# Kernel tuning notes

Measured on AMD Instinct MI355X. Metric: run time of the kernel, lower is better.

Reference implementation:

```python
import jax, jax.numpy as jnp
import numpy as np

# hyperparameters (from hp_manager)
UNTANH = 3.0
W_SCALE = 4.0
EMA_SPEED = 0.01
REW_SENS = 4.0
NOISE_SCALE = 0.01
WD = 1e-4
SPEED = 1.0
WIDTH = 4.0
MOMENTUM = 0.9
LR = 0.01
C_MOMENT = 0.9
A_VAR_GOAL = 0.01
BUNTANH_SCALE = float(np.sqrt(2.0 + np.sqrt(2.0)))
B, N, D = 4, 512, 128


def rms_norm(x, axes=(-1,), eps=1e-8):
    return x * jax.lax.rsqrt(jnp.mean(x * x, axis=axes, keepdims=True) + eps)


def buntanh(x, a, s):
    return a * jnp.tanh(x / a) * s


def sinkhorn_knopp(A, n_iters=5, eps=1e-6):
    for _ in range(n_iters):
        A = A / (jnp.sum(A, axis=-1, keepdims=True) + eps)
        A = A / (jnp.sum(A, axis=-2, keepdims=True) + eps)
    return A


def wrapping_gaussian_mask(dim, center, width):
    j = jnp.arange(dim, dtype=jnp.float32)
    d = jnp.abs(j - center)
    d = jnp.minimum(d, dim - d)  # wrap-around distance
    return jnp.exp(-(d * d) / (2.0 * width * width))


def piece_forward(x, W):
    raw = jnp.einsum('bnj,bnjk->bnk', x, W)
    return buntanh(raw, UNTANH, BUNTANH_SCALE)


def piece_gradient(layer_input, err, E_base, key):
    E_curr = jax.nn.softmax(err, axis=-1)
    E_new = E_base * (1.0 - EMA_SPEED) + EMA_SPEED * E_curr
    advantage = E_curr - E_new
    plasticity = 1.0 + rms_norm(advantage[..., None] * REW_SENS)  # [B,N,D,1]
    noisy = layer_input + NOISE_SCALE * jax.random.normal(key, layer_input.shape, layer_input.dtype)
    lg1 = rms_norm(-(err[..., :, None] * noisy[..., None, :]))  # bni,bnj->bnij
    return plasticity * lg1, E_new


def piece_step(W, g_ema, grad, step_counter):
    grad = grad - WD * W
    center = (step_counter * SPEED) % D
    mask = wrapping_gaussian_mask(D, center, WIDTH)  # applied along last dim
    grad = grad * mask
    g_new = MOMENTUM * g_ema + (1.0 - MOMENTUM) * grad
    W_new = W + LR * g_new
    W_new = rms_norm(W_new, axes=(-1, -2)) * W_SCALE
    return W_new, g_new


def setup_inputs() -> dict:
    key = jax.random.key(0)
    ks = jax.random.split(key, 14)
    return {
        'state': 1e-5 * jax.random.normal(ks[0], (B, N, D), jnp.float32),
        'output': 1e-5 * jax.random.normal(ks[1], (B, N, D), jnp.float32),
        'A_ema': jax.random.normal(ks[2], (B, N, N), jnp.float32),
        'w1': jax.random.normal(ks[3], (B, N, D, D), jnp.float32) / np.sqrt(D),
        'w2': jax.random.normal(ks[4], (B, N, D, D), jnp.float32) / np.sqrt(D),
        'w3': jax.random.normal(ks[5], (B, N, D, D), jnp.float32) / np.sqrt(D),
        'g1': 0.01 * jax.random.normal(ks[6], (B, N, D, D), jnp.float32),
        'g2': 0.01 * jax.random.normal(ks[7], (B, N, D, D), jnp.float32),
        'g3': 0.01 * jax.random.normal(ks[8], (B, N, D, D), jnp.float32),
        'eb1': 0.01 + 0.01 * jax.random.normal(ks[9], (B, N, D), jnp.float32),
        'eb2': 0.01 + 0.01 * jax.random.normal(ks[10], (B, N, D), jnp.float32),
        'eb3': 0.01 + 0.01 * jax.random.normal(ks[11], (B, N, D), jnp.float32),
        'eye_env': jax.random.normal(ks[12], (B, D), jnp.float32),
        'stomach_env': jax.random.normal(ks[13], (B, D), jnp.float32),
        'step_counter': 2,
    }


def reference(state, output, A_ema, w1, w2, w3, g1, g2, g3, eb1, eb2, eb3,
              eye_env, stomach_env, step_counter):
    sg = jax.lax.stop_gradient
    nkey = jax.random.key(1)
    k_bore, k1, k2, k3 = jax.random.split(nkey, 4)

    queries = piece_forward(state, w3)
    keys = piece_forward(state, w2)
    prediction = piece_forward(state, w1)

    raw_A = jnp.einsum('bnd,bmd->bnm', queries, keys) / np.sqrt(D)
    raw_A = rms_norm(raw_A, axes=(-1, -2))
    if step_counter == 1:
        A_ema_new = raw_A
    else:
        A_ema_new = A_ema * C_MOMENT + raw_A * (1.0 - C_MOMENT)
    raw_A = sinkhorn_knopp(A_ema_new)
    uniform_baseline = 0.5 / N
    sparse_A = jnp.where(raw_A > uniform_baseline, raw_A, 0.0)
    A = sinkhorn_knopp(sparse_A)
    A = A.at[:, 0:2, :].set(0.0)

    current_var = jnp.var(A, axis=(-1, -2), keepdims=True)  # [B,1,1]
    vd = jax.nn.relu(A_VAR_GOAL - current_var)
    boredom_noise = vd * jax.random.normal(k_bore, output.shape, output.dtype)
    target = jnp.einsum('bnm,bmd->bnd', A, output + boredom_noise)
    target = target.at[:, 0, :].set(eye_env).at[:, 1, :].set(stomach_env)

    err1_base = prediction - target
    err2 = keys - sg(err1_base)
    err3 = queries - sg(err2)
    err1 = prediction - (target + sg(err3))

    gr1, eb1n = piece_gradient(state, err1, eb1, k1)
    gr2, eb2n = piece_gradient(state, err2, eb2, k2)
    gr3, eb3n = piece_gradient(state, err3, eb3, k3)
    w1n, g1n = piece_step(w1, g1, gr1, step_counter)
    w2n, g2n = piece_step(w2, g2, gr2, step_counter)
    w3n, g3n = piece_step(w3, g3, gr3, step_counter)

    new_output = prediction
    new_state = target
    return (new_state, new_output, w1n, w2n, w3n, A_ema_new)
```

## Files before the change

kernel.cpp:

```cpp
#include <hip/hip_runtime.h>
#include <math.h>

#define Bq 4
#define Nq 512
#define Dq 128

#define C_UNTANH   3.0f
#define C_BSCALE   1.8477590650225735f
#define C_INVSQRTD 0.08838834764831845f
#define C_WD       1e-4f
#define C_MOM      0.9f
#define C_LR       0.01f
#define C_WSCALE   4.0f

__global__ __launch_bounds__(256) void k_fwd(const float* __restrict__ state,
    const float* __restrict__ w1, const float* __restrict__ w2, const float* __restrict__ w3,
    float* __restrict__ pred, float* __restrict__ keyv, float* __restrict__ qry) {
  int bn = blockIdx.x;
  int t = threadIdx.x;
  int k = t & 127;
  int half = t >> 7;
  __shared__ float xs[Dq];
  __shared__ float ps[256];
  if (t < Dq) xs[t] = state[bn * Dq + t];
  __syncthreads();
  const float* Ws[3] = {w1, w2, w3};
  float* dsts[3] = {pred, keyv, qry};
  for (int p = 0; p < 3; p++) {
    const float* W = Ws[p] + (size_t)bn * Dq * Dq + (size_t)half * 64 * Dq;
    float acc = 0.f;
#pragma unroll 16
    for (int j = 0; j < 64; j++) acc += xs[half * 64 + j] * W[j * Dq + k];
    ps[t] = acc;
    __syncthreads();
    if (t < Dq) {
      float r = ps[t] + ps[t + 128];
      r = C_UNTANH * tanhf(r / C_UNTANH) * C_BSCALE;
      dsts[p][bn * Dq + t] = r;
    }
    __syncthreads();
  }
}

__global__ __launch_bounds__(256) void k_qk(const float* __restrict__ qry,
    const float* __restrict__ keyv, float* __restrict__ rawS, double* __restrict__ part) {
  __shared__ float Qs[16][Dq + 1];
  __shared__ float Ks[16][Dq + 1];
  __shared__ double red[256];
  int b = blockIdx.z, n0 = blockIdx.x * 16, m0 = blockIdx.y * 16;
  int t = threadIdx.x;
#pragma unroll
  for (int i = 0; i < 8; i++) {
    int idx = i * 256 + t;
    int r = idx >> 7, c = idx & 127;
    Qs[r][c] = qry[((size_t)b * Nq + n0 + r) * Dq + c];
    Ks[r][c] = keyv[((size_t)b * Nq + m0 + r) * Dq + c];
  }
  __syncthreads();
  int tn = t >> 4, tm = t & 15;
  float a = 0.f;
#pragma unroll 16
  for (int d = 0; d < Dq; d++) a += Qs[tn][d] * Ks[tm][d];
  a *= C_INVSQRTD;
  rawS[((size_t)b * Nq + n0 + tn) * Nq + m0 + tm] = a;
  red[t] = (double)a * (double)a;
  __syncthreads();
  for (int s = 128; s > 0; s >>= 1) { if (t < s) red[t] += red[t + s]; __syncthreads(); }
  if (t == 0) part[(size_t)b * 1024 + blockIdx.y * 32 + blockIdx.x] = red[0];
}

__global__ __launch_bounds__(256) void k_acc(const double* __restrict__ part, double* __restrict__ acc) {
  int b = blockIdx.x, t = threadIdx.x;
  double s = 0.0;
  for (int i = t; i < 1024; i += 256) s += part[(size_t)b * 1024 + i];
  __shared__ double red[256];
  red[t] = s;
  __syncthreads();
  for (int k = 128; k > 0; k >>= 1) { if (t < k) red[t] += red[t + k]; __syncthreads(); }
  if (t == 0) acc[b] = red[0];
}

__global__ __launch_bounds__(256) void k_ema(float* __restrict__ A, const float* __restrict__ A_ema,
    const double* __restrict__ acc, const int* __restrict__ stepc, float* __restrict__ outA) {
  int idx = blockIdx.x * 256 + threadIdx.x;
  if (idx >= Bq * Nq * Nq) return;
  int b = idx / (Nq * Nq);
  float mean = (float)(acc[b] / (double)(Nq * Nq));
  float rs = 1.0f / sqrtf(mean + 1e-8f);
  float val = A[idx] * rs;
  float res = (stepc[0] == 1) ? val : 0.9f * A_ema[idx] + 0.1f * val;
  outA[idx] = res;
  A[idx] = res;
}

__global__ __launch_bounds__(256) void k_row(float* __restrict__ A) {
  int bn = blockIdx.x, t = threadIdx.x;
  float* row = A + (size_t)bn * Nq;
  float v0 = row[t], v1 = row[t + 256];
  __shared__ double red[256];
  red[t] = (double)v0 + (double)v1;
  __syncthreads();
  for (int s = 128; s > 0; s >>= 1) { if (t < s) red[t] += red[t + s]; __syncthreads(); }
  double den = red[0] + 1e-6;
  row[t] = (float)((double)v0 / den);
  row[t + 256] = (float)((double)v1 / den);
}

__global__ __launch_bounds__(256) void k_col(float* __restrict__ A) {
  int blk = blockIdx.x, t = threadIdx.x;
  int b = blk >> 9, m = blk & 511;
  float* base = A + (size_t)b * Nq * Nq + m;
  float v0 = base[(size_t)t * Nq], v1 = base[(size_t)(t + 256) * Nq];
  __shared__ double red[256];
  red[t] = (double)v0 + (double)v1;
  __syncthreads();
  for (int s = 128; s > 0; s >>= 1) { if (t < s) red[t] += red[t + s]; __syncthreads(); }
  double den = red[0] + 1e-6;
  base[(size_t)t * Nq] = (float)((double)v0 / den);
  base[(size_t)(t + 256) * Nq] = (float)((double)v1 / den);
}

__global__ __launch_bounds__(256) void k_sparse(float* __restrict__ A) {
  int idx = blockIdx.x * 256 + threadIdx.x;
  if (idx >= Bq * Nq * Nq) return;
  float v = A[idx];
  A[idx] = (v > 0.0009765625f) ? v : 0.0f;
}

__global__ __launch_bounds__(128) void k_target(const float* __restrict__ A,
    const float* __restrict__ output, const float* __restrict__ eye_env,
    const float* __restrict__ stomach_env, float* __restrict__ out_state) {
  int bn = blockIdx.x, t = threadIdx.x;
  int b = bn >> 9, n = bn & 511;
  float tg;
  if (n == 0) {
    tg = eye_env[b * Dq + t];
  } else if (n == 1) {
    tg = stomach_env[b * Dq + t];
  } else {
    const float* Arow = A + (size_t)bn * Nq;
    const float* ob = output + (size_t)b * Nq * Dq;
    __shared__ float as[128];
    float acc = 0.f;
    for (int m0 = 0; m0 < Nq; m0 += 128) {
      __syncthreads();
      as[t] = Arow[m0 + t];
      __syncthreads();
#pragma unroll 16
      for (int m = 0; m < 128; m++) acc += as[m] * ob[(size_t)(m0 + m) * Dq + t];
    }
    tg = acc;
  }
  out_state[(size_t)bn * Dq + t] = tg;
}

__device__ __forceinline__ void softmax_plast(float e, const float* __restrict__ eb,
    float* __restrict__ pl, int base, int t, float* red) {
  red[t] = e;
  __syncthreads();
  for (int s = 64; s > 0; s >>= 1) { if (t < s) red[t] = fmaxf(red[t], red[t + s]); __syncthreads(); }
  float mx = red[0];
  __syncthreads();
  float ex = expf(e - mx);
  red[t] = ex;
  __syncthreads();
  for (int s = 64; s > 0; s >>= 1) { if (t < s) red[t] += red[t + s]; __syncthreads(); }
  float Ec = ex / red[0];
  __syncthreads();
  float En = eb[base] * 0.99f + 0.01f * Ec;
  float adv = Ec - En;
  float x = adv * 4.0f;
  pl[base] = 1.0f + x / sqrtf(x * x + 1e-8f);
}

__global__ __launch_bounds__(128) void k_err(const float* __restrict__ pred,
    const float* __restrict__ qry, const float* __restrict__ keyv,
    const float* __restrict__ target, const float* __restrict__ state,
    const float* __restrict__ eb1, const float* __restrict__ eb2, const float* __restrict__ eb3,
    float* __restrict__ err1, float* __restrict__ err2, float* __restrict__ err3,
    float* __restrict__ pl1, float* __restrict__ pl2, float* __restrict__ pl3,
    float* __restrict__ msn) {
  int bn = blockIdx.x, t = threadIdx.x;
  int base = bn * Dq + t;
  float pr = pred[base], qv = qry[base], kv = keyv[base], tg = target[base];
  float e1b = pr - tg;
  float e2 = kv - e1b;
  float e3 = qv - e2;
  float e1 = pr - (tg + e3);
  err1[base] = e1; err2[base] = e2; err3[base] = e3;
  __shared__ float red[128];
  float st = state[base];
  red[t] = st * st;
  __syncthreads();
  for (int s = 64; s > 0; s >>= 1) { if (t < s) red[t] += red[t + s]; __syncthreads(); }
  if (t == 0) msn[bn] = red[0] / (float)Dq;
  __syncthreads();
  softmax_plast(e1, eb1, pl1, base, t, red);
  softmax_plast(e2, eb2, pl2, base, t, red);
  softmax_plast(e3, eb3, pl3, base, t, red);
}

__device__ __forceinline__ float stepw(float w, float g, float c, float st, float mk, double* ssq) {
  float grad = (c * st - C_WD * w) * mk;
  float gn = C_MOM * g + (1.0f - C_MOM) * grad;
  float wn = w + C_LR * gn;
  *ssq += (double)wn * (double)wn;
  return wn;
}

__global__ __launch_bounds__(256) void k_step(const float* __restrict__ W, const float* __restrict__ G,
    const float* __restrict__ err, const float* __restrict__ pl, const float* __restrict__ state,
    const float* __restrict__ msn, const int* __restrict__ stepc, float* __restrict__ outW) {
  int bn = blockIdx.x, t = threadIdx.x;
  __shared__ __align__(16) float Wn[Dq * Dq];
  __shared__ __align__(16) float ers[Dq];
  __shared__ __align__(16) float pls[Dq];
  __shared__ __align__(16) float sts[Dq];
  __shared__ __align__(16) float msk[Dq];
  __shared__ double red[256];
  if (t < Dq) {
    ers[t] = err[bn * Dq + t];
    pls[t] = pl[bn * Dq + t];
    sts[t] = state[bn * Dq + t];
    float center = fmodf((float)stepc[0] * 1.0f, 128.0f);
    float d = fabsf((float)t - center);
    d = fminf(d, 128.0f - d);
    msk[t] = expf(-(d * d) * (1.0f / 32.0f));
  }
  float msnv = msn[bn];
  __syncthreads();
  const float4* W4 = (const float4*)(W + (size_t)bn * Dq * Dq);
  const float4* G4 = (const float4*)(G + (size_t)bn * Dq * Dq);
  float4* Wn4 = (float4*)Wn;
  double ssq = 0.0;
#pragma unroll
  for (int i = 0; i < 16; i++) {
    int f4 = i * 256 + t;
    int p = f4 >> 5;
    float4 w4v = W4[f4];
    float4 g4v = G4[f4];
    float4 st4 = ((const float4*)sts)[f4 & 31];
    float4 mk4 = ((const float4*)msk)[f4 & 31];
    float ep = ers[p];
    float denom = sqrtf(ep * ep * msnv + 1e-8f);
    float c = -pls[p] * ep / denom;
    float4 o;
    o.x = stepw(w4v.x, g4v.x, c, st4.x, mk4.x, &ssq);
    o.y = stepw(w4v.y, g4v.y, c, st4.y, mk4.y, &ssq);
    o.z = stepw(w4v.z, g4v.z, c, st4.z, mk4.z, &ssq);
    o.w = stepw(w4v.w, g4v.w, c, st4.w, mk4.w, &ssq);
    Wn4[f4] = o;
  }
  red[t] = ssq;
  __syncthreads();
  for (int s = 128; s > 0; s >>= 1) { if (t < s) red[t] += red[t + s]; __syncthreads(); }
  float mean = (float)(red[0] / (double)(Dq * Dq));
  float scale = C_WSCALE / sqrtf(mean + 1e-8f);
  float4* out4 = (float4*)(outW + (size_t)bn * Dq * Dq);
#pragma unroll
  for (int i = 0; i < 16; i++) {
    int f4 = i * 256 + t;
    float4 v = Wn4[f4];
    v.x *= scale; v.y *= scale; v.z *= scale; v.w *= scale;
    out4[f4] = v;
  }
}

extern "C" void kernel_launch(void* const* d_in, const int* in_sizes, int n_in,
                              void* d_out, int out_size, void* d_ws, size_t ws_size,
                              hipStream_t stream) {
  const float* state   = (const float*)d_in[0];
  const float* output  = (const float*)d_in[1];
  const float* A_ema   = (const float*)d_in[2];
  const float* w1      = (const float*)d_in[3];
  const float* w2      = (const float*)d_in[4];
  const float* w3      = (const float*)d_in[5];
  const float* g1      = (const float*)d_in[6];
  const float* g2      = (const float*)d_in[7];
  const float* g3      = (const float*)d_in[8];
  const float* eb1     = (const float*)d_in[9];
  const float* eb2     = (const float*)d_in[10];
  const float* eb3     = (const float*)d_in[11];
  const float* eye     = (const float*)d_in[12];
  const float* stomach = (const float*)d_in[13];
  const int*   stepc   = (const int*)d_in[14];

  float* out = (float*)d_out;
  float* o_state = out;
  float* o_out   = out + 262144;
  float* o_w1    = out + 524288;
  float* o_w2    = o_w1 + 33554432;
  float* o_w3    = o_w2 + 33554432;
  float* o_A     = o_w3 + 33554432;

  float* ws = (float*)d_ws;
  float* A    = ws;
  float* qry  = ws + 1048576;
  float* keyv = ws + 1310720;
  float* err1 = ws + 1572864;
  float* err2 = ws + 1835008;
  float* err3 = ws + 2097152;
  float* pl1  = ws + 2359296;
  float* pl2  = ws + 2621440;
  float* pl3  = ws + 2883584;
  float* msn  = ws + 3145728;
  double* part = (double*)(ws + 3147776);
  double* acc  = part + 4096;

  k_fwd<<<Bq * Nq, 256, 0, stream>>>(state, w1, w2, w3, o_out, keyv, qry);
  k_qk<<<dim3(32, 32, Bq), 256, 0, stream>>>(qry, keyv, A, part);
  k_acc<<<Bq, 256, 0, stream>>>(part, acc);
  k_ema<<<4096, 256, 0, stream>>>(A, A_ema, acc, stepc, o_A);
  for (int it = 0; it < 5; it++) {
    k_row<<<Bq * Nq, 256, 0, stream>>>(A);
    k_col<<<Bq * Nq, 256, 0, stream>>>(A);
  }
  k_sparse<<<4096, 256, 0, stream>>>(A);
  for (int it = 0; it < 5; it++) {
    k_row<<<Bq * Nq, 256, 0, stream>>>(A);
    k_col<<<Bq * Nq, 256, 0, stream>>>(A);
  }
  k_target<<<Bq * Nq, 128, 0, stream>>>(A, output, eye, stomach, o_state);
  k_err<<<Bq * Nq, 128, 0, stream>>>(o_out, qry, keyv, o_state, state,
                                     eb1, eb2, eb3, err1, err2, err3, pl1, pl2, pl3, msn);
  k_step<<<Bq * Nq, 256, 0, stream>>>(w1, g1, err1, pl1, state, msn, stepc, o_w1);
  k_step<<<Bq * Nq, 256, 0, stream>>>(w2, g2, err2, pl2, state, msn, stepc, o_w2);
  k_step<<<Bq * Nq, 256, 0, stream>>>(w3, g3, err3, pl3, state, msn, stepc, o_w3);
}
```

Baseline: 1.286 ms.

## Fuse Sinkhorn pipeline into cooperative kernel and restructure fwd, target, step kernels

Replaces the EMA, sparsify and twenty row/column normalization launches with one cooperative kernel. It keeps each block's column slab in registers and exchanges partial row sums through global memory with grid syncs. It also vectorizes the forward matvec and QK dot products with float4, and retiles the target matmul to compute several rows per block from a shared output tile. The three weight-step kernels become one launch that holds the updated weights in registers instead of shared memory. This cuts launch count and global traffic on A, but only 64 blocks run the Sinkhorn phase and normalization moves from double to float precision.

```diff
diff --git a/kernel.cpp b/kernel.cpp
--- a/kernel.cpp
+++ b/kernel.cpp
@@ -1,5 +1,8 @@
 #include <hip/hip_runtime.h>
+#include <hip/hip_cooperative_groups.h>
 #include <math.h>
+
+namespace cg = cooperative_groups;
 
 #define Bq 4
 #define Nq 512
@@ -12,30 +15,39 @@
 #define C_MOM      0.9f
 #define C_LR       0.01f
 #define C_WSCALE   4.0f
+#define C_SPARSE   0.0009765625f
 
 __global__ __launch_bounds__(256) void k_fwd(const float* __restrict__ state,
     const float* __restrict__ w1, const float* __restrict__ w2, const float* __restrict__ w3,
     float* __restrict__ pred, float* __restrict__ keyv, float* __restrict__ qry) {
   int bn = blockIdx.x;
   int t = threadIdx.x;
-  int k = t & 127;
-  int half = t >> 7;
+  int g = t & 31;
+  int h = t >> 5;
   __shared__ float xs[Dq];
-  __shared__ float ps[256];
+  __shared__ float4 red[8][32];
   if (t < Dq) xs[t] = state[bn * Dq + t];
   __syncthreads();
   const float* Ws[3] = {w1, w2, w3};
   float* dsts[3] = {pred, keyv, qry};
   for (int p = 0; p < 3; p++) {
-    const float* W = Ws[p] + (size_t)bn * Dq * Dq + (size_t)half * 64 * Dq;
-    float acc = 0.f;
-#pragma unroll 16
-    for (int j = 0; j < 64; j++) acc += xs[half * 64 + j] * W[j * Dq + k];
-    ps[t] = acc;
+    const float4* W4 = (const float4*)(Ws[p] + (size_t)bn * Dq * Dq);
+    float4 acc = {0.f, 0.f, 0.f, 0.f};
+#pragma unroll
+    for (int i = 0; i < 16; i++) {
+      int j = h * 16 + i;
+      float x = xs[j];
+      float4 w = W4[j * 32 + g];
+      acc.x += x * w.x; acc.y += x * w.y; acc.z += x * w.z; acc.w += x * w.w;
+    }
+    red[h][g] = acc;
     __syncthreads();
     if (t < Dq) {
-      float r = ps[t] + ps[t + 128];
-      r = C_UNTANH * tanhf(r / C_UNTANH) * C_BSCALE;
+      const float* rp = (const float*)&red[0][0];
+      float ssum = 0.f;
+#pragma unroll
+      for (int h2 = 0; h2 < 8; h2++) ssum += rp[h2 * 128 + t];
+      float r = C_UNTANH * tanhf(ssum / C_UNTANH) * C_BSCALE;
       dsts[p][bn * Dq + t] = r;
     }
     __syncthreads();
@@ -44,8 +56,8 @@
 
 __global__ __launch_bounds__(256) void k_qk(const float* __restrict__ qry,
     const float* __restrict__ keyv, float* __restrict__ rawS, double* __restrict__ part) {
-  __shared__ float Qs[16][Dq + 1];
-  __shared__ float Ks[16][Dq + 1];
+  __shared__ float Qs[16][132];
+  __shared__ float Ks[16][132];
   __shared__ double red[256];
   int b = blockIdx.z, n0 = blockIdx.x * 16, m0 = blockIdx.y * 16;
   int t = threadIdx.x;
@@ -58,9 +70,15 @@
   }
   __syncthreads();
   int tn = t >> 4, tm = t & 15;
+  const float4* Q4 = (const float4*)&Qs[tn][0];
+  const float4* K4 = (const float4*)&Ks[tm][0];
   float a = 0.f;
-#pragma unroll 16
-  for (int d = 0; d < Dq; d++) a += Qs[tn][d] * Ks[tm][d];
+#pragma unroll
+  for (int d = 0; d < 32; d++) {
+    float4 q = Q4[d];
+    float4 k = K4[d];
+    a += q.x * k.x + q.y * k.y + q.z * k.z + q.w * k.w;
+  }
   a *= C_INVSQRTD;
   rawS[((size_t)b * Nq + n0 + tn) * Nq + m0 + tm] = a;
   red[t] = (double)a * (double)a;
@@ -69,89 +87,158 @@
   if (t == 0) part[(size_t)b * 1024 + blockIdx.y * 32 + blockIdx.x] = red[0];
 }
 
-__global__ __launch_bounds__(256) void k_acc(const double* __restrict__ part, double* __restrict__ acc) {
-  int b = blockIdx.x, t = threadIdx.x;
-  double s = 0.0;
-  for (int i = t; i < 1024; i += 256) s += part[(size_t)b * 1024 + i];
-  __shared__ double red[256];
-  red[t] = s;
-  __syncthreads();
-  for (int k = 128; k > 0; k >>= 1) { if (t < k) red[t] += red[t + k]; __syncthreads(); }
-  if (t == 0) acc[b] = red[0];
-}
-
-__global__ __launch_bounds__(256) void k_ema(float* __restrict__ A, const float* __restrict__ A_ema,
-    const double* __restrict__ acc, const int* __restrict__ stepc, float* __restrict__ outA) {
-  int idx = blockIdx.x * 256 + threadIdx.x;
-  if (idx >= Bq * Nq * Nq) return;
-  int b = idx / (Nq * Nq);
-  float mean = (float)(acc[b] / (double)(Nq * Nq));
-  float rs = 1.0f / sqrtf(mean + 1e-8f);
-  float val = A[idx] * rs;
-  float res = (stepc[0] == 1) ? val : 0.9f * A_ema[idx] + 0.1f * val;
-  outA[idx] = res;
-  A[idx] = res;
-}
-
-__global__ __launch_bounds__(256) void k_row(float* __restrict__ A) {
-  int bn = blockIdx.x, t = threadIdx.x;
-  float* row = A + (size_t)bn * Nq;
-  float v0 = row[t], v1 = row[t + 256];
-  __shared__ double red[256];
-  red[t] = (double)v0 + (double)v1;
-  __syncthreads();
-  for (int s = 128; s > 0; s >>= 1) { if (t < s) red[t] += red[t + s]; __syncthreads(); }
-  double den = red[0] + 1e-6;
-  row[t] = (float)((double)v0 / den);
-  row[t + 256] = (float)((double)v1 / den);
-}
-
-__global__ __launch_bounds__(256) void k_col(float* __restrict__ A) {
-  int blk = blockIdx.x, t = threadIdx.x;
-  int b = blk >> 9, m = blk & 511;
-  float* base = A + (size_t)b * Nq * Nq + m;
-  float v0 = base[(size_t)t * Nq], v1 = base[(size_t)(t + 256) * Nq];
-  __shared__ double red[256];
-  red[t] = (double)v0 + (double)v1;
-  __syncthreads();
-  for (int s = 128; s > 0; s >>= 1) { if (t < s) red[t] += red[t + s]; __syncthreads(); }
-  double den = red[0] + 1e-6;
-  base[(size_t)t * Nq] = (float)((double)v0 / den);
-  base[(size_t)(t + 256) * Nq] = (float)((double)v1 / den);
-}
-
-__global__ __launch_bounds__(256) void k_sparse(float* __restrict__ A) {
-  int idx = blockIdx.x * 256 + threadIdx.x;
-  if (idx >= Bq * Nq * Nq) return;
-  float v = A[idx];
-  A[idx] = (v > 0.0009765625f) ? v : 0.0f;
-}
-
-__global__ __launch_bounds__(128) void k_target(const float* __restrict__ A,
+__global__ __launch_bounds__(256) void k_Apipe(float* __restrict__ A,
+    const float* __restrict__ A_ema, const double* __restrict__ part,
+    const int* __restrict__ stepc, float* __restrict__ outA, float* __restrict__ prs) {
+  cg::grid_group grid = cg::this_grid();
+  int blk = blockIdx.x;
+  int b = blk >> 4;
+  int s = blk & 15;
+  int m0 = s * 32;
+  int t = threadIdx.x;
+  int c4 = t & 7;
+  int rq = t >> 3;
+  __shared__ float rs_l[512];
+  __shared__ float cs_l[32];
+  __shared__ float4 carr[32][8];
+  __shared__ double dred[256];
+
+  double ps = 0.0;
+  for (int i = t; i < 1024; i += 256) ps += part[(size_t)b * 1024 + i];
+  dred[t] = ps;
+  __syncthreads();
+  for (int k = 128; k > 0; k >>= 1) { if (t < k) dred[t] += dred[t + k]; __syncthreads(); }
+  float invs = rsqrtf((float)(dred[0] / (double)(Nq * Nq)) + 1e-8f);
+  int step1 = (stepc[0] == 1);
+
+  const size_t brow = (size_t)b * Nq;
+  float4 vS[16];
+
+#pragma unroll
+  for (int k = 0; k < 16; k++) {
+    int r = rq + 32 * k;
+    const float4* Ar = (const float4*)(A + (brow + r) * Nq + m0);
+    float4 v = Ar[c4];
+    v.x *= invs; v.y *= invs; v.z *= invs; v.w *= invs;
+    if (!step1) {
+      const float4* Er = (const float4*)(A_ema + (brow + r) * Nq + m0);
+      float4 e = Er[c4];
+      v.x = 0.9f * e.x + 0.1f * v.x;
+      v.y = 0.9f * e.y + 0.1f * v.y;
+      v.z = 0.9f * e.z + 0.1f * v.z;
+      v.w = 0.9f * e.w + 0.1f * v.w;
+    }
+    vS[k] = v;
+    float4* Or = (float4*)(outA + (brow + r) * Nq + m0);
+    Or[c4] = v;
+    float p = v.x + v.y + v.z + v.w;
+    p += __shfl_xor(p, 1);
+    p += __shfl_xor(p, 2);
+    p += __shfl_xor(p, 4);
+    if (c4 == 0) prs[((size_t)(b * 16 + s)) * 512 + r] = p;
+  }
+  __threadfence();
+  grid.sync();
+
+  for (int iter = 0; iter < 10; iter++) {
+    for (int r = t; r < 512; r += 256) {
+      float ssum = 0.f;
+#pragma unroll
+      for (int s2 = 0; s2 < 16; s2++) ssum += prs[((size_t)(b * 16 + s2)) * 512 + r];
+      rs_l[r] = 1.0f / (ssum + 1e-6f);
+    }
+    __syncthreads();
+    float4 cacc = {0.f, 0.f, 0.f, 0.f};
+#pragma unroll
+    for (int k = 0; k < 16; k++) {
+      int r = rq + 32 * k;
+      float rv = rs_l[r];
+      float4 v = vS[k];
+      v.x *= rv; v.y *= rv; v.z *= rv; v.w *= rv;
+      vS[k] = v;
+      cacc.x += v.x; cacc.y += v.y; cacc.z += v.z; cacc.w += v.w;
+    }
+    carr[rq][c4] = cacc;
+    __syncthreads();
+    if (t < 32) {
+      const float* cf = (const float*)&carr[0][0];
+      float ssum = 0.f;
+#pragma unroll
+      for (int q = 0; q < 32; q++) ssum += cf[q * 32 + t];
+      cs_l[t] = 1.0f / (ssum + 1e-6f);
+    }
+    __syncthreads();
+    float4 cm = ((const float4*)cs_l)[c4];
+    int last = (iter == 9);
+#pragma unroll
+    for (int k = 0; k < 16; k++) {
+      int r = rq + 32 * k;
+      float4 v = vS[k];
+      v.x *= cm.x; v.y *= cm.y; v.z *= cm.z; v.w *= cm.w;
+      if (iter == 4) {
+        v.x = (v.x > C_SPARSE) ? v.x : 0.f;
+        v.y = (v.y > C_SPARSE) ? v.y : 0.f;
+        v.z = (v.z > C_SPARSE) ? v.z : 0.f;
+        v.w = (v.w > C_SPARSE) ? v.w : 0.f;
+      }
+      vS[k] = v;
+      if (!last) {
+        float p = v.x + v.y + v.z + v.w;
+        p += __shfl_xor(p, 1);
+        p += __shfl_xor(p, 2);
+        p += __shfl_xor(p, 4);
+        if (c4 == 0) prs[((size_t)(b * 16 + s)) * 512 + r] = p;
+      } else {
+        float4* Ar = (float4*)(A + (brow + r) * Nq + m0);
+        Ar[c4] = v;
+      }
+    }
+    if (!last) {
+      __threadfence();
+      grid.sync();
+      __syncthreads();
+    }
+  }
+}
+
+__global__ __launch_bounds__(256) void k_target(const float* __restrict__ A,
     const float* __restrict__ output, const float* __restrict__ eye_env,
     const float* __restrict__ stomach_env, float* __restrict__ out_state) {
-  int bn = blockIdx.x, t = threadIdx.x;
-  int b = bn >> 9, n = bn & 511;
-  float tg;
-  if (n == 0) {
-    tg = eye_env[b * Dq + t];
-  } else if (n == 1) {
-    tg = stomach_env[b * Dq + t];
-  } else {
-    const float* Arow = A + (size_t)bn * Nq;
-    const float* ob = output + (size_t)b * Nq * Dq;
-    __shared__ float as[128];
-    float acc = 0.f;
-    for (int m0 = 0; m0 < Nq; m0 += 128) {
-      __syncthreads();
-      as[t] = Arow[m0 + t];
-      __syncthreads();
-#pragma unroll 16
-      for (int m = 0; m < 128; m++) acc += as[m] * ob[(size_t)(m0 + m) * Dq + t];
-    }
-    tg = acc;
-  }
-  out_state[(size_t)bn * Dq + t] = tg;
+  int blk = blockIdx.x;
+  int b = blk >> 7;
+  int n0 = (blk & 127) * 4;
+  int t = threadIdx.x;
+  int tr = t >> 7;
+  int c = t & 127;
+  __shared__ float as[4][Nq];
+  __shared__ float tile[64][Dq];
+  const float4* Ab4 = (const float4*)(A + ((size_t)b * Nq + n0) * Nq);
+  float4* as4 = (float4*)&as[0][0];
+  as4[t] = Ab4[t];
+  as4[t + 256] = Ab4[t + 256];
+  float acc0 = 0.f, acc1 = 0.f;
+  const float4* ob4 = (const float4*)(output + (size_t)b * Nq * Dq);
+  for (int m0 = 0; m0 < Nq; m0 += 64) {
+    __syncthreads();
+    float4* t4 = (float4*)&tile[0][0];
+    const float4* src = ob4 + m0 * 32;
+#pragma unroll
+    for (int i = 0; i < 8; i++) t4[i * 256 + t] = src[i * 256 + t];
+    __syncthreads();
+#pragma unroll 8
+    for (int m = 0; m < 64; m++) {
+      float ov = tile[m][c];
+      acc0 += as[tr][m0 + m] * ov;
+      acc1 += as[tr + 2][m0 + m] * ov;
+    }
+  }
+  int na = n0 + tr;
+  int nb = na + 2;
+  float v0 = acc0;
+  if (na == 0) v0 = eye_env[b * Dq + c];
+  if (na == 1) v0 = stomach_env[b * Dq + c];
+  out_state[((size_t)b * Nq + na) * Dq + c] = v0;
+  out_state[((size_t)b * Nq + nb) * Dq + c] = acc1;
 }
 
 __device__ __forceinline__ void softmax_plast(float e, const float* __restrict__ eb,
@@ -208,11 +295,21 @@
   return wn;
 }
 
-__global__ __launch_bounds__(256) void k_step(const float* __restrict__ W, const float* __restrict__ G,
-    const float* __restrict__ err, const float* __restrict__ pl, const float* __restrict__ state,
-    const float* __restrict__ msn, const int* __restrict__ stepc, float* __restrict__ outW) {
-  int bn = blockIdx.x, t = threadIdx.x;
-  __shared__ __align__(16) float Wn[Dq * Dq];
+__global__ __launch_bounds__(256) void k_step3(
+    const float* __restrict__ w1, const float* __restrict__ w2, const float* __restrict__ w3,
+    const float* __restrict__ g1, const float* __restrict__ g2, const float* __restrict__ g3,
+    const float* __restrict__ err1, const float* __restrict__ err2, const float* __restrict__ err3,
+    const float* __restrict__ pl1, const float* __restrict__ pl2, const float* __restrict__ pl3,
+    const float* __restrict__ state, const float* __restrict__ msn, const int* __restrict__ stepc,
+    float* __restrict__ ow1, float* __restrict__ ow2, float* __restrict__ ow3) {
+  int p = blockIdx.x >> 11;
+  int bn = blockIdx.x & 2047;
+  const float* W   = (p == 0) ? w1 : (p == 1) ? w2 : w3;
+  const float* G   = (p == 0) ? g1 : (p == 1) ? g2 : g3;
+  const float* err = (p == 0) ? err1 : (p == 1) ? err2 : err3;
+  const float* pl  = (p == 0) ? pl1 : (p == 1) ? pl2 : pl3;
+  float* outW      = (p == 0) ? ow1 : (p == 1) ? ow2 : ow3;
+  int t = threadIdx.x;
   __shared__ __align__(16) float ers[Dq];
   __shared__ __align__(16) float pls[Dq];
   __shared__ __align__(16) float sts[Dq];
@@ -222,7 +319,7 @@
     ers[t] = err[bn * Dq + t];
     pls[t] = pl[bn * Dq + t];
     sts[t] = state[bn * Dq + t];
-    float center = fmodf((float)stepc[0] * 1.0f, 128.0f);
+    float center = fmodf((float)stepc[0], 128.0f);
     float d = fabsf((float)t - center);
     d = fminf(d, 128.0f - d);
     msk[t] = expf(-(d * d) * (1.0f / 32.0f));
@@ -231,36 +328,36 @@
   __syncthreads();
   const float4* W4 = (const float4*)(W + (size_t)bn * Dq * Dq);
   const float4* G4 = (const float4*)(G + (size_t)bn * Dq * Dq);
-  float4* Wn4 = (float4*)Wn;
+  float4 wn[16];
   double ssq = 0.0;
 #pragma unroll
   for (int i = 0; i < 16; i++) {
     int f4 = i * 256 + t;
-    int p = f4 >> 5;
+    int row = f4 >> 5;
     float4 w4v = W4[f4];
     float4 g4v = G4[f4];
     float4 st4 = ((const float4*)sts)[f4 & 31];
     float4 mk4 = ((const float4*)msk)[f4 & 31];
-    float ep = ers[p];
+    float ep = ers[row];
     float denom = sqrtf(ep * ep * msnv + 1e-8f);
-    float c = -pls[p] * ep / denom;
+    float c = -pls[row] * ep / denom;
     float4 o;
     o.x = stepw(w4v.x, g4v.x, c, st4.x, mk4.x, &ssq);
     o.y = stepw(w4v.y, g4v.y, c, st4.y, mk4.y, &ssq);
     o.z = stepw(w4v.z, g4v.z, c, st4.z, mk4.z, &ssq);
     o.w = stepw(w4v.w, g4v.w, c, st4.w, mk4.w, &ssq);
-    Wn4[f4] = o;
+    wn[i] = o;
   }
   red[t] = ssq;
   __syncthreads();
-  for (int s = 128; s > 0; s >>= 1) { if (t < s) red[t] += red[t + s]; __syncthreads(); }
+  for (int k = 128; k > 0; k >>= 1) { if (t < k) red[t] += red[t + k]; __syncthreads(); }
   float mean = (float)(red[0] / (double)(Dq * Dq));
   float scale = C_WSCALE / sqrtf(mean + 1e-8f);
   float4* out4 = (float4*)(outW + (size_t)bn * Dq * Dq);
 #pragma unroll
   for (int i = 0; i < 16; i++) {
     int f4 = i * 256 + t;
-    float4 v = Wn4[f4];
+    float4 v = wn[i];
     v.x *= scale; v.y *= scale; v.z *= scale; v.w *= scale;
     out4[f4] = v;
   }
@@ -305,25 +402,24 @@
   float* pl3  = ws + 2883584;
   float* msn  = ws + 3145728;
   double* part = (double*)(ws + 3147776);
-  double* acc  = part + 4096;
+  float* prs  = err1;
 
   k_fwd<<<Bq * Nq, 256, 0, stream>>>(state, w1, w2, w3, o_out, keyv, qry);
   k_qk<<<dim3(32, 32, Bq), 256, 0, stream>>>(qry, keyv, A, part);
-  k_acc<<<Bq, 256, 0, stream>>>(part, acc);
-  k_ema<<<4096, 256, 0, stream>>>(A, A_ema, acc, stepc, o_A);
-  for (int it = 0; it < 5; it++) {
-    k_row<<<Bq * Nq, 256, 0, stream>>>(A);
-    k_col<<<Bq * Nq, 256, 0, stream>>>(A);
-  }
-  k_sparse<<<4096, 256, 0, stream>>>(A);
-  for (int it = 0; it < 5; it++) {
-    k_row<<<Bq * Nq, 256, 0, stream>>>(A);
-    k_col<<<Bq * Nq, 256, 0, stream>>>(A);
-  }
-  k_target<<<Bq * Nq, 128, 0, stream>>>(A, output, eye, stomach, o_state);
+  {
+    float* A_ = A;
+    const float* Aema_ = A_ema;
+    const double* part_ = part;
+    const int* stepc_ = stepc;
+    float* oA_ = o_A;
+    float* prs_ = prs;
+    void* args[] = {&A_, &Aema_, &part_, &stepc_, &oA_, &prs_};
+    hipLaunchCooperativeKernel((void*)k_Apipe, dim3(Bq * 16), dim3(256), args, 0, stream);
+  }
+  k_target<<<Bq * 128, 256, 0, stream>>>(A, output, eye, stomach, o_state);
   k_err<<<Bq * Nq, 128, 0, stream>>>(o_out, qry, keyv, o_state, state,
                                      eb1, eb2, eb3, err1, err2, err3, pl1, pl2, pl3, msn);
-  k_step<<<Bq * Nq, 256, 0, stream>>>(w1, g1, err1, pl1, state, msn, stepc, o_w1);
-  k_step<<<Bq * Nq, 256, 0, stream>>>(w2, g2, err2, pl2, state, msn, stepc, o_w2);
-  k_step<<<Bq * Nq, 256, 0, stream>>>(w3, g3, err3, pl3, state, msn, stepc, o_w3);
-}
+  k_step3<<<3 * Bq * Nq, 256, 0, stream>>>(w1, w2, w3, g1, g2, g3,
+                                           err1, err2, err3, pl1, pl2, pl3,
+                                           state, msn, stepc, o_w1, o_w2, o_w3);
+}
```

Measured after the change: 1.303 ms. Within noise of the previous version (+1.4%).
